# Kernel tuning notes

Hardware: AMD Instinct MI355X
Metric: run time of the kernel (lower is better)

The kernel has to match this reference:

```python
import jax, jax.numpy as jnp
import numpy as np

N = 5000
E = 80000
EPS = 1e-3


def setup_inputs() -> dict:
    key = jax.random.key(0)
    ks = jax.random.split(key, 12)
    inp = {
        'x': jax.random.normal(ks[0], (N, 35), jnp.float32),
        'edge_index': jax.random.randint(ks[1], (2, E), 0, N, jnp.int64),
        'edge_attr': jax.random.uniform(ks[2], (E, 1), jnp.float32),
        'W1': jax.random.normal(ks[3], (1, 1225), jnp.float32) * 0.1,
        'b1': jax.random.normal(ks[4], (1225,), jnp.float32) * 0.1,
        'root1': jax.random.normal(ks[5], (35, 35), jnp.float32) * 0.1,
        'bias1': jax.random.normal(ks[6], (35,), jnp.float32) * 0.1,
        'g1': jnp.ones((35,), jnp.float32),
        'be1': jnp.zeros((35,), jnp.float32),
        'rm1': jnp.zeros((35,), jnp.float32),
        'rv1': jnp.ones((35,), jnp.float32),
        'W3': jax.random.normal(ks[7], (1, 5600), jnp.float32) * 0.1,
        'b3': jax.random.normal(ks[8], (5600,), jnp.float32) * 0.1,
        'root3': jax.random.normal(ks[9], (35, 160), jnp.float32) * 0.1,
        'bias3': jax.random.normal(ks[10], (160,), jnp.float32) * 0.1,
        'g3': jnp.ones((160,), jnp.float32),
        'be3': jnp.zeros((160,), jnp.float32),
        'rm3': jnp.zeros((160,), jnp.float32),
        'rv3': jnp.ones((160,), jnp.float32),
    }
    return inp


def nnconv(x, edge_index, edge_attr, Wm, bm, root, bias, in_ch, out_ch):
    # edge-MLP generates per-edge weight matrices [E, in_ch, out_ch]
    theta = jax.nn.relu(edge_attr @ Wm + bm).reshape(-1, in_ch, out_ch)
    src, dst = edge_index[0], edge_index[1]
    msg = jnp.einsum('ei,eio->eo', x[src], theta)  # per-edge matmul
    summ = jax.ops.segment_sum(msg, dst, num_segments=N)
    cnt = jax.ops.segment_sum(jnp.ones((msg.shape[0],), x.dtype), dst, num_segments=N)
    mean = summ / jnp.maximum(cnt, 1.0)[:, None]  # scatter-mean (0 for isolated nodes)
    return mean + x @ root + bias


def batchnorm_eval(x, g, b, rm, rv):
    return (x - rm) * (g * jax.lax.rsqrt(rv + EPS)) + b


def reference(x, edge_index, edge_attr, W1, b1, root1, bias1, g1, be1, rm1, rv1,
              W3, b3, root3, bias3, g3, be3, rm3, rv3):
    h1 = nnconv(x, edge_index, edge_attr, W1, b1, root1, bias1, 35, 35)
    x1 = jax.nn.sigmoid(batchnorm_eval(h1, g1, be1, rm1, rv1))
    # dropout is identity in eval mode
    h3 = nnconv(x1, edge_index, edge_attr, W3, b3, root3, bias3, 35, 160)
    x3 = jax.nn.sigmoid(batchnorm_eval(h3, g3, be3, rm3, rv3))
    return x3.T @ x3  # [160, 160]
```

## Files before the change

### kernel.cpp

```cpp
#include <hip/hip_runtime.h>
#include <math.h>

#define NN 5000
#define NE 80000
#define EPSB 1e-3f
#define GZ 100

__device__ __forceinline__ unsigned int f2bf(float f) {
    unsigned int u = __float_as_uint(f);
    return (u + 0x7FFFu + ((u >> 16) & 1u)) >> 16;
}
__device__ __forceinline__ float bf2f(unsigned short h) {
    return __uint_as_float(((unsigned int)h) << 16);
}


__global__ void k_prep(const float* __restrict__ x, float* __restrict__ x_p,
                       const int* __restrict__ ei, int* __restrict__ counts) {
    int t = blockIdx.x * 256 + threadIdx.x;
    if (t < NN * 36) {
        int n = t / 36, i = t - n * 36;
        x_p[t] = (i < 35) ? x[n * 35 + i] : 0.f;
    }
    if (t < NE) atomicAdd(&counts[ei[NE + t]], 1);
}

__global__ void k_scan(const int* __restrict__ counts, int* __restrict__ offs) {
    __shared__ int ps[256];
    int t = threadIdx.x;
    int base = t * 20;
    int loc[20];
    int s = 0;
#pragma unroll
    for (int j = 0; j < 20; ++j) {
        int idx = base + j;
        int v = (idx < NN) ? counts[idx] : 0;
        loc[j] = s; s += v;
    }
    ps[t] = s;
    __syncthreads();
    for (int off = 1; off < 256; off <<= 1) {
        int v = (t >= off) ? ps[t - off] : 0;
        __syncthreads();
        ps[t] += v;
        __syncthreads();
    }
    int pre = (t > 0) ? ps[t - 1] : 0;
#pragma unroll
    for (int j = 0; j < 20; ++j) {
        int idx = base + j;
        if (idx < NN) offs[idx] = pre + loc[j];
    }
    if (t == 255) offs[NN] = ps[255];
}

__global__ void k_fill(const int* __restrict__ ei, const int* __restrict__ offs,
                       int* __restrict__ cursor, int* __restrict__ eslot) {
    int e = blockIdx.x * blockDim.x + threadIdx.x;
    if (e >= NE) return;
    int dst = ei[NE + e];
    int p = atomicAdd(&cursor[dst], 1);
    eslot[e] = offs[dst] + p;
}


__global__ __launch_bounds__(256) void k_edge1(
    const int* __restrict__ ei, const float* __restrict__ ea,
    const int* __restrict__ eslot,
    const float* __restrict__ x_p,
    const float* __restrict__ W1, const float* __restrict__ b1,
    unsigned short* __restrict__ msg1)
{
    __shared__ float wls[36][36];
    __shared__ float bls[36][36];
    for (int idx = threadIdx.x; idx < 1296; idx += 256) {
        int i = idx / 36, o = idx - i * 36;
        bool in = (i < 35) && (o < 35);
        wls[i][o] = in ? W1[i * 35 + o] : 0.f;
        bls[i][o] = in ? b1[i * 35 + o] : 0.f;
    }
    __syncthreads();
    int e = blockIdx.x * 256 + threadIdx.x;
    if (e >= NE) return;
    int src = ei[e];
    float a = ea[e];
    const float4* xp4 = (const float4*)(x_p + src * 36);
    float acc[36];
#pragma unroll
    for (int o = 0; o < 36; ++o) acc[o] = 0.f;
    float4 xv = xp4[0];
#pragma unroll 1
    for (int q = 0; q < 9; ++q) {
        float4 xn = (q < 8) ? xp4[q + 1] : xv;
        float xs4[4] = {xv.x, xv.y, xv.z, xv.w};
#pragma unroll
        for (int r = 0; r < 4; ++r) {
            int i = q * 4 + r;
            float xvr = xs4[r];
            const float4* wr = (const float4*)(&wls[i][0]);
            const float4* br = (const float4*)(&bls[i][0]);
#pragma unroll
            for (int oq = 0; oq < 9; ++oq) {
                float4 wv = wr[oq], bv = br[oq];
                int o0 = oq * 4;
                acc[o0 + 0] = fmaf(xvr, fmaxf(0.f, fmaf(a, wv.x, bv.x)), acc[o0 + 0]);
                acc[o0 + 1] = fmaf(xvr, fmaxf(0.f, fmaf(a, wv.y, bv.y)), acc[o0 + 1]);
                acc[o0 + 2] = fmaf(xvr, fmaxf(0.f, fmaf(a, wv.z, bv.z)), acc[o0 + 2]);
                acc[o0 + 3] = fmaf(xvr, fmaxf(0.f, fmaf(a, wv.w, bv.w)), acc[o0 + 3]);
            }
        }
        xv = xn;
    }
    unsigned int pk[18];
#pragma unroll
    for (int k = 0; k < 18; ++k)
        pk[k] = f2bf(acc[2 * k]) | (f2bf(acc[2 * k + 1]) << 16);
    uint2* dst = (uint2*)(msg1 + (size_t)eslot[e] * 36);
#pragma unroll
    for (int j = 0; j < 9; ++j) dst[j] = make_uint2(pk[2 * j], pk[2 * j + 1]);
}


__global__ __launch_bounds__(256) void k_sum1(
    const int* __restrict__ offs,
    const unsigned short* __restrict__ msg1,
    const float* __restrict__ x_p,
    const float* __restrict__ root1, const float* __restrict__ bias1,
    const float* __restrict__ g, const float* __restrict__ be,
    const float* __restrict__ rm, const float* __restrict__ rv,
    float* __restrict__ x1p)
{
    int t = blockIdx.x * 256 + threadIdx.x;
    if (t >= NN * 36) return;
    int n = t / 36, o = t - n * 36;
    if (o == 35) { x1p[t] = 0.f; return; }
    int off = offs[n];
    int deg = offs[n + 1] - off;
    const unsigned short* base = msg1 + (size_t)off * 36 + o;
    float s = 0.f;
    for (int j = 0; j < deg; ++j) s += bf2f(base[(size_t)j * 36]);
    float mean = s / fmaxf((float)deg, 1.0f);
    float r = 0.f;
#pragma unroll 7
    for (int i = 0; i < 35; ++i) r = fmaf(x_p[n * 36 + i], root1[i * 35 + o], r);
    float h = mean + r + bias1[o];
    float z = (h - rm[o]) * (g[o] * rsqrtf(rv[o] + EPSB)) + be[o];
    x1p[t] = 1.f / (1.f + expf(-z));
}


__global__ __launch_bounds__(256) void k_edge3(
    const int* __restrict__ ei, const float* __restrict__ ea,
    const int* __restrict__ eslot,
    const float* __restrict__ x1p,
    const float* __restrict__ W3, const float* __restrict__ b3,
    unsigned short* __restrict__ msg3)
{
    __shared__ float wls[36][32];
    __shared__ float bls[36][32];
    int ob = blockIdx.y * 32;
    for (int idx = threadIdx.x; idx < 1152; idx += 256) {
        int i = idx >> 5, o = idx & 31;
        bool in = (i < 35);
        wls[i][o] = in ? W3[i * 160 + ob + o] : 0.f;
        bls[i][o] = in ? b3[i * 160 + ob + o] : 0.f;
    }
    __syncthreads();
    int e = blockIdx.x * 256 + threadIdx.x;
    if (e >= NE) return;
    int src = ei[e];
    float a = ea[e];
    const float4* xp4 = (const float4*)(x1p + src * 36);
    float acc[32];
#pragma unroll
    for (int o = 0; o < 32; ++o) acc[o] = 0.f;
    float4 xv = xp4[0];
#pragma unroll 1
    for (int q = 0; q < 9; ++q) {
        float4 xn = (q < 8) ? xp4[q + 1] : xv;
        float xs4[4] = {xv.x, xv.y, xv.z, xv.w};
#pragma unroll
        for (int r = 0; r < 4; ++r) {
            int i = q * 4 + r;
            float xvr = xs4[r];
            const float4* wr = (const float4*)(&wls[i][0]);
            const float4* br = (const float4*)(&bls[i][0]);
#pragma unroll
            for (int oq = 0; oq < 8; ++oq) {
                float4 wv = wr[oq], bv = br[oq];
                int o0 = oq * 4;
                acc[o0 + 0] = fmaf(xvr, fmaxf(0.f, fmaf(a, wv.x, bv.x)), acc[o0 + 0]);
                acc[o0 + 1] = fmaf(xvr, fmaxf(0.f, fmaf(a, wv.y, bv.y)), acc[o0 + 1]);
                acc[o0 + 2] = fmaf(xvr, fmaxf(0.f, fmaf(a, wv.z, bv.z)), acc[o0 + 2]);
                acc[o0 + 3] = fmaf(xvr, fmaxf(0.f, fmaf(a, wv.w, bv.w)), acc[o0 + 3]);
            }
        }
        xv = xn;
    }
    unsigned int pk[16];
#pragma unroll
    for (int k = 0; k < 16; ++k)
        pk[k] = f2bf(acc[2 * k]) | (f2bf(acc[2 * k + 1]) << 16);
    uint4* dst = (uint4*)(msg3 + ((size_t)blockIdx.y * NE + eslot[e]) * 32);
#pragma unroll
    for (int j = 0; j < 4; ++j)
        dst[j] = make_uint4(pk[4 * j], pk[4 * j + 1], pk[4 * j + 2], pk[4 * j + 3]);
}


__global__ __launch_bounds__(320) void k_sum3(
    const int* __restrict__ offs,
    const unsigned short* __restrict__ msg3,
    const float* __restrict__ x1p,
    const float* __restrict__ root3, const float* __restrict__ bias3,
    const float* __restrict__ g, const float* __restrict__ be,
    const float* __restrict__ rm, const float* __restrict__ rv,
    float* __restrict__ x3)
{
    __shared__ float xn[4][36];
    int tid = threadIdx.x;
    int g_ = tid / 80;
    int o2 = tid - g_ * 80;
    int o  = o2 * 2;
    int n  = blockIdx.x * 4 + g_;
    if (tid < 144) xn[tid / 36][tid % 36] = x1p[(blockIdx.x * 4 + tid / 36) * 36 + tid % 36];
    __syncthreads();
    int off = offs[n];
    int deg = offs[n + 1] - off;
    int chunk = o >> 5, oo = o & 31;
    const unsigned short* base = msg3 + ((size_t)chunk * NE + off) * 32 + oo;
    float s0 = 0.f, s1 = 0.f;
    for (int j = 0; j < deg; ++j) {
        unsigned int u = *(const unsigned int*)(base + (size_t)j * 32);
        s0 += bf2f((unsigned short)(u & 0xffff));
        s1 += bf2f((unsigned short)(u >> 16));
    }
    float inv = 1.f / fmaxf((float)deg, 1.0f);
    float m0 = s0 * inv, m1 = s1 * inv;
    float r0 = 0.f, r1 = 0.f;
#pragma unroll 7
    for (int i = 0; i < 35; ++i) {
        float xvi = xn[g_][i];
        r0 = fmaf(xvi, root3[i * 160 + o], r0);
        r1 = fmaf(xvi, root3[i * 160 + o + 1], r1);
    }
    float h0 = m0 + r0 + bias3[o];
    float h1 = m1 + r1 + bias3[o + 1];
    float z0 = (h0 - rm[o]) * (g[o] * rsqrtf(rv[o] + EPSB)) + be[o];
    float z1 = (h1 - rm[o + 1]) * (g[o + 1] * rsqrtf(rv[o + 1] + EPSB)) + be[o + 1];
    float2 res = make_float2(1.f / (1.f + expf(-z0)), 1.f / (1.f + expf(-z1)));
    *(float2*)(x3 + n * 160 + o) = res;
}


__global__ void k_gram(const float* __restrict__ x3, float* __restrict__ part) {
    int tx = threadIdx.x, ty = threadIdx.y;
    int i = blockIdx.x * 64 + tx * 4;
    int j = blockIdx.y * 64 + ty * 4;
    if (i >= 160 || j >= 160) return;
    int k0 = blockIdx.z * 50;
    float acc[4][4];
#pragma unroll
    for (int r = 0; r < 4; ++r)
#pragma unroll
        for (int c = 0; c < 4; ++c) acc[r][c] = 0.f;
#pragma unroll 5
    for (int k = k0; k < k0 + 50; ++k) {
        float4 av = *(const float4*)&x3[k * 160 + i];
        float4 bv = *(const float4*)&x3[k * 160 + j];
        float ar[4] = {av.x, av.y, av.z, av.w};
        float br[4] = {bv.x, bv.y, bv.z, bv.w};
#pragma unroll
        for (int r = 0; r < 4; ++r)
#pragma unroll
            for (int c = 0; c < 4; ++c) acc[r][c] = fmaf(ar[r], br[c], acc[r][c]);
    }
    float* pp = part + (size_t)blockIdx.z * 25600;
#pragma unroll
    for (int r = 0; r < 4; ++r)
#pragma unroll
        for (int c = 0; c < 4; ++c) pp[(i + r) * 160 + (j + c)] = acc[r][c];
}

__global__ void k_reduce(const float* __restrict__ part, float* __restrict__ out) {
    int t = blockIdx.x * 256 + threadIdx.x;
    if (t >= 25600) return;
    float s = 0.f;
#pragma unroll 10
    for (int z = 0; z < GZ; ++z) s += part[(size_t)z * 25600 + t];
    out[t] = s;
}


extern "C" void kernel_launch(void* const* d_in, const int* in_sizes, int n_in,
                              void* d_out, int out_size, void* d_ws, size_t ws_size,
                              hipStream_t stream) {
    const float* x     = (const float*)d_in[0];
    const int*   ei    = (const int*)d_in[1];
    const float* ea    = (const float*)d_in[2];
    const float* W1    = (const float*)d_in[3];
    const float* b1    = (const float*)d_in[4];
    const float* root1 = (const float*)d_in[5];
    const float* bias1 = (const float*)d_in[6];
    const float* g1    = (const float*)d_in[7];
    const float* be1   = (const float*)d_in[8];
    const float* rm1   = (const float*)d_in[9];
    const float* rv1   = (const float*)d_in[10];
    const float* W3    = (const float*)d_in[11];
    const float* b3    = (const float*)d_in[12];
    const float* root3 = (const float*)d_in[13];
    const float* bias3 = (const float*)d_in[14];
    const float* g3    = (const float*)d_in[15];
    const float* be3   = (const float*)d_in[16];
    const float* rm3   = (const float*)d_in[17];
    const float* rv3   = (const float*)d_in[18];
    float* out = (float*)d_out;

    char* wsb = (char*)d_ws;
    int*   counts = (int*)(wsb + 0);
    int*   cursor = (int*)(wsb + 20480);
    int*   offs   = (int*)(wsb + 40960);
    int*   eslot  = (int*)(wsb + 61440);
    float* x_p    = (float*)(wsb + 381952);
    float* x1p    = (float*)(wsb + 1101952);
    float* x3     = (float*)(wsb + 1821952);
    unsigned short* msg1 = (unsigned short*)(wsb + 5021952);
    unsigned short* msg3 = (unsigned short*)(wsb + 10781952);
    float* part   = (float*)(wsb + 10781952);

    hipMemsetAsync(d_ws, 0, (size_t)2 * 5120 * sizeof(int), stream);

    int eb = (NE + 255) / 256;
    k_prep <<<(NN * 36 + 255) / 256, 256, 0, stream>>>(x, x_p, ei, counts);
    k_scan <<<1, 256, 0, stream>>>(counts, offs);
    k_fill <<<eb, 256, 0, stream>>>(ei, offs, cursor, eslot);
    k_edge1<<<eb, 256, 0, stream>>>(ei, ea, eslot, x_p, W1, b1, msg1);
    k_sum1 <<<(NN * 36 + 255) / 256, 256, 0, stream>>>(offs, msg1, x_p,
                                                       root1, bias1, g1, be1, rm1, rv1, x1p);
    k_edge3<<<dim3(eb, 5), 256, 0, stream>>>(ei, ea, eslot, x1p, W3, b3, msg3);
    k_sum3 <<<1250, 320, 0, stream>>>(offs, msg3, x1p,
                                      root3, bias3, g3, be3, rm3, rv3, x3);
    k_gram <<<dim3(3, 3, GZ), dim3(16, 16), 0, stream>>>(x3, part);
    k_reduce<<<(25600 + 255) / 256, 256, 0, stream>>>(part, out);
}
```

Before: 240.1 us.

## Fuse CSR slot fill into edge1 and read edge-MLP weights via scalar loads

```diff
diff --git a/kernel.cpp b/kernel.cpp
--- a/kernel.cpp
+++ b/kernel.cpp
@@ -54,70 +54,52 @@
     if (t == 255) offs[NN] = ps[255];
 }
 
-__global__ void k_fill(const int* __restrict__ ei, const int* __restrict__ offs,
-                       int* __restrict__ cursor, int* __restrict__ eslot) {
-    int e = blockIdx.x * blockDim.x + threadIdx.x;
-    if (e >= NE) return;
-    int dst = ei[NE + e];
-    int p = atomicAdd(&cursor[dst], 1);
-    eslot[e] = offs[dst] + p;
-}
-
 
 __global__ __launch_bounds__(256) void k_edge1(
     const int* __restrict__ ei, const float* __restrict__ ea,
-    const int* __restrict__ eslot,
+    const int* __restrict__ offs, int* __restrict__ cursor,
+    int* __restrict__ eslot,
     const float* __restrict__ x_p,
     const float* __restrict__ W1, const float* __restrict__ b1,
     unsigned short* __restrict__ msg1)
 {
-    __shared__ float wls[36][36];
-    __shared__ float bls[36][36];
-    for (int idx = threadIdx.x; idx < 1296; idx += 256) {
-        int i = idx / 36, o = idx - i * 36;
-        bool in = (i < 35) && (o < 35);
-        wls[i][o] = in ? W1[i * 35 + o] : 0.f;
-        bls[i][o] = in ? b1[i * 35 + o] : 0.f;
-    }
-    __syncthreads();
     int e = blockIdx.x * 256 + threadIdx.x;
     if (e >= NE) return;
+    int dst = ei[NE + e];
+    int p = atomicAdd(&cursor[dst], 1);
+    int slot = offs[dst] + p;
+    eslot[e] = slot;
+
     int src = ei[e];
     float a = ea[e];
     const float4* xp4 = (const float4*)(x_p + src * 36);
     float acc[36];
 #pragma unroll
     for (int o = 0; o < 36; ++o) acc[o] = 0.f;
-    float4 xv = xp4[0];
-#pragma unroll 1
+#pragma unroll
     for (int q = 0; q < 9; ++q) {
-        float4 xn = (q < 8) ? xp4[q + 1] : xv;
+        float4 xv = xp4[q];
         float xs4[4] = {xv.x, xv.y, xv.z, xv.w};
 #pragma unroll
         for (int r = 0; r < 4; ++r) {
             int i = q * 4 + r;
-            float xvr = xs4[r];
-            const float4* wr = (const float4*)(&wls[i][0]);
-            const float4* br = (const float4*)(&bls[i][0]);
-#pragma unroll
-            for (int oq = 0; oq < 9; ++oq) {
-                float4 wv = wr[oq], bv = br[oq];
-                int o0 = oq * 4;
-                acc[o0 + 0] = fmaf(xvr, fmaxf(0.f, fmaf(a, wv.x, bv.x)), acc[o0 + 0]);
-                acc[o0 + 1] = fmaf(xvr, fmaxf(0.f, fmaf(a, wv.y, bv.y)), acc[o0 + 1]);
-                acc[o0 + 2] = fmaf(xvr, fmaxf(0.f, fmaf(a, wv.z, bv.z)), acc[o0 + 2]);
-                acc[o0 + 3] = fmaf(xvr, fmaxf(0.f, fmaf(a, wv.w, bv.w)), acc[o0 + 3]);
-            }
+            if (i >= 35) continue;
+            float xi = xs4[r];
+            const float* wr = W1 + i * 35;
+            const float* br = b1 + i * 35;
+#pragma unroll
+            for (int o = 0; o < 35; ++o)
+                acc[o] = fmaf(xi, fmaxf(0.f, fmaf(a, wr[o], br[o])), acc[o]);
         }
-        xv = xn;
-    }
+    }
+    acc[35] = 0.f;
     unsigned int pk[18];
 #pragma unroll
     for (int k = 0; k < 18; ++k)
         pk[k] = f2bf(acc[2 * k]) | (f2bf(acc[2 * k + 1]) << 16);
-    uint2* dst = (uint2*)(msg1 + (size_t)eslot[e] * 36);
-#pragma unroll
-    for (int j = 0; j < 9; ++j) dst[j] = make_uint2(pk[2 * j], pk[2 * j + 1]);
+    uint2* dstp = (uint2*)(msg1 + (size_t)slot * 36);
+#pragma unroll
+    for (int j = 0; j < 9; ++j) dstp[j] = make_uint2(pk[2 * j], pk[2 * j + 1]);
 }
 
 
@@ -156,46 +138,31 @@
     const float* __restrict__ W3, const float* __restrict__ b3,
     unsigned short* __restrict__ msg3)
 {
-    __shared__ float wls[36][32];
-    __shared__ float bls[36][32];
-    int ob = blockIdx.y * 32;
-    for (int idx = threadIdx.x; idx < 1152; idx += 256) {
-        int i = idx >> 5, o = idx & 31;
-        bool in = (i < 35);
-        wls[i][o] = in ? W3[i * 160 + ob + o] : 0.f;
-        bls[i][o] = in ? b3[i * 160 + ob + o] : 0.f;
-    }
-    __syncthreads();
     int e = blockIdx.x * 256 + threadIdx.x;
     if (e >= NE) return;
+    const float* Wb = W3 + blockIdx.y * 32;
+    const float* Bb = b3 + blockIdx.y * 32;
     int src = ei[e];
     float a = ea[e];
     const float4* xp4 = (const float4*)(x1p + src * 36);
     float acc[32];
 #pragma unroll
     for (int o = 0; o < 32; ++o) acc[o] = 0.f;
-    float4 xv = xp4[0];
-#pragma unroll 1
+#pragma unroll
     for (int q = 0; q < 9; ++q) {
-        float4 xn = (q < 8) ? xp4[q + 1] : xv;
+        float4 xv = xp4[q];
         float xs4[4] = {xv.x, xv.y, xv.z, xv.w};
 #pragma unroll
         for (int r = 0; r < 4; ++r) {
             int i = q * 4 + r;
-            float xvr = xs4[r];
-            const float4* wr = (const float4*)(&wls[i][0]);
-            const float4* br = (const float4*)(&bls[i][0]);
-#pragma unroll
-            for (int oq = 0; oq < 8; ++oq) {
-                float4 wv = wr[oq], bv = br[oq];
-                int o0 = oq * 4;
-                acc[o0 + 0] = fmaf(xvr, fmaxf(0.f, fmaf(a, wv.x, bv.x)), acc[o0 + 0]);
-                acc[o0 + 1] = fmaf(xvr, fmaxf(0.f, fmaf(a, wv.y, bv.y)), acc[o0 + 1]);
-                acc[o0 + 2] = fmaf(xvr, fmaxf(0.f, fmaf(a, wv.z, bv.z)), acc[o0 + 2]);
-                acc[o0 + 3] = fmaf(xvr, fmaxf(0.f, fmaf(a, wv.w, bv.w)), acc[o0 + 3]);
-            }
+            if (i >= 35) continue;
+            float xi = xs4[r];
+            const float* wr = Wb + i * 160;
+            const float* br = Bb + i * 160;
+#pragma unroll
+            for (int o = 0; o < 32; ++o)
+                acc[o] = fmaf(xi, fmaxf(0.f, fmaf(a, wr[o], br[o])), acc[o]);
         }
-        xv = xn;
     }
     unsigned int pk[16];
 #pragma unroll
@@ -333,8 +300,7 @@
     int eb = (NE + 255) / 256;
     k_prep <<<(NN * 36 + 255) / 256, 256, 0, stream>>>(x, x_p, ei, counts);
     k_scan <<<1, 256, 0, stream>>>(counts, offs);
-    k_fill <<<eb, 256, 0, stream>>>(ei, offs, cursor, eslot);
-    k_edge1<<<eb, 256, 0, stream>>>(ei, ea, eslot, x_p, W1, b1, msg1);
+    k_edge1<<<eb, 256, 0, stream>>>(ei, ea, offs, cursor, eslot, x_p, W1, b1, msg1);
     k_sum1 <<<(NN * 36 + 255) / 256, 256, 0, stream>>>(offs, msg1, x_p,
                                                        root1, bias1, g1, be1, rm1, rv1, x1p);
     k_edge3<<<dim3(eb, 5), 256, 0, stream>>>(ei, ea, eslot, x1p, W3, b3, msg3);
```

Result: slower. 263.5 us (+9.7%).
